# Optimization experiments

Measured on AMD Instinct MI355X. Metric: run time of the kernel, lower is better.

The kernel has to match this reference:

```python
import jax, jax.numpy as jnp
import numpy as np

N = 30000
E = 480000
VDIM = 512
HID = 32
EPS_BN = 1e-5
EPS_COS = 1e-8


def setup_inputs() -> dict:
    key = jax.random.key(0)
    ks = jax.random.split(key, 12)
    inp = {}
    inp["x"] = jax.random.normal(ks[0], (N, 2), dtype=jnp.float32)
    inp["visual"] = jax.random.normal(ks[1], (N, VDIM), dtype=jnp.float32)
    inp["edge_index"] = jax.random.randint(ks[2], (2, E), 0, N, dtype=jnp.int64)
    # input_mlp: Linear(2,32) -> BN(32) -> PReLU -> Dropout(0) -> Linear(32,32)
    inp["w1"] = jax.random.normal(ks[3], (HID, 2), dtype=jnp.float32) * 0.1
    inp["b1"] = jnp.zeros((HID,), dtype=jnp.float32)
    inp["gamma"] = jnp.ones((HID,), dtype=jnp.float32)
    inp["beta"] = jnp.zeros((HID,), dtype=jnp.float32)
    inp["prelu_a"] = jnp.asarray(0.25, dtype=jnp.float32)  # torch default: single shared slope
    inp["w2"] = jax.random.normal(ks[4], (HID, HID), dtype=jnp.float32) * 0.1
    inp["b2"] = jnp.zeros((HID,), dtype=jnp.float32)
    # CMCosConv(32, 32, 512): linear over cos-weighted mean aggregation
    inp["wc"] = jax.random.normal(ks[5], (HID, HID), dtype=jnp.float32) * 0.1
    inp["bc"] = jnp.zeros((HID,), dtype=jnp.float32)
    # gcn_projection_face: Linear(32,1)
    inp["wp"] = jax.random.normal(ks[6], (1, HID), dtype=jnp.float32) * 0.1
    inp["bp"] = jnp.zeros((1,), dtype=jnp.float32)
    return inp


def reference(x, visual, edge_index, w1, b1, gamma, beta, prelu_a, w2, b2, wc, bc, wp, bp):
    # ---- input_mlp ----
    h = x @ w1.T + b1  # [N,32]
    mu = jnp.mean(h, axis=0)
    var = jnp.mean((h - mu) ** 2, axis=0)  # biased, training-mode BN
    h = (h - mu) * jax.lax.rsqrt(var + EPS_BN) * gamma + beta
    h = jnp.where(h >= 0, h, prelu_a * h)  # PReLU, single slope
    h = h @ w2.T + b2  # [N,32]

    # ---- CMCosConv: edge weight = cos(visual_src, visual_dst); cos-weighted mean agg; linear ----
    vn = visual / jnp.maximum(jnp.linalg.norm(visual, axis=-1, keepdims=True), EPS_COS)  # [N,512]
    src = edge_index[0]
    dst = edge_index[1]
    w = jnp.sum(vn[src] * vn[dst], axis=-1)  # [E] cosine per edge (memory-bound gathers)
    msg = w[:, None] * h[src]  # [E,32]
    agg = jax.ops.segment_sum(msg, dst, num_segments=N)  # [N,32]
    deg = jax.ops.segment_sum(jnp.ones_like(w), dst, num_segments=N)  # [N]
    agg = agg / jnp.maximum(deg, 1.0)[:, None]  # mean aggregation
    hc = agg @ wc.T + bc  # [N,32]; conv_activation=None -> identity

    # ---- projection ----
    scores = (hc @ wp.T + bp).squeeze(-1)  # [N]
    return scores
```

## Files before the change

kernel.cpp:

```cpp
#include <hip/hip_runtime.h>
#include <hip/hip_fp16.h>
#include <math.h>

#define N_NODES 30000
#define E_EDGES 480000
#define VD      512
#define HID     32
#define BUCKET  3750
#define K1_BLOCKS 512

#define ACC_OFF  0
#define DEG_OFF  30000
#define SARR_OFF 60000
#define PART_OFF 90000
#define INV_OFF  92560
#define NV_BYTE_OFF 524288u

__device__ inline int edot4(unsigned int a, unsigned int b, int c) {
#if __has_builtin(__builtin_amdgcn_sdot4)
    return __builtin_amdgcn_sdot4((int)a, (int)b, (int)c, false);
#else
    int r = c;
    r += (int)(signed char)(a)       * (int)(signed char)(b);
    r += (int)(signed char)(a >> 8)  * (int)(signed char)(b >> 8);
    r += (int)(signed char)(a >> 16) * (int)(signed char)(b >> 16);
    r += (int)(signed char)(a >> 24) * (int)(signed char)(b >> 24);
    return r;
#endif
}

__device__ inline unsigned int pack4i8(float x0, float x1, float x2, float x3, float sc) {
    int q0 = (int)rintf(x0 * sc);
    int q1 = (int)rintf(x1 * sc);
    int q2 = (int)rintf(x2 * sc);
    int q3 = (int)rintf(x3 * sc);
    return (unsigned int)(q0 & 255) | ((unsigned int)(q1 & 255) << 8) |
           ((unsigned int)(q2 & 255) << 16) | ((unsigned int)(q3 & 255) << 24);
}

__global__ void __launch_bounds__(256) k1_prep(
        const float* __restrict__ x,
        const float* __restrict__ visual,
        float* __restrict__ ws, int i8mode) {
    const int t      = threadIdx.x;
    const int gid    = blockIdx.x * blockDim.x + t;
    const int stride = gridDim.x * blockDim.x;
    const int lane   = t & 63;

    for (int i = gid; i < 2 * N_NODES; i += stride) ws[i] = 0.f;

    {
        __shared__ float red[4][5];
        float s0 = 0.f, s1 = 0.f, s00 = 0.f, s11 = 0.f, s01 = 0.f;
        for (int i = gid; i < N_NODES; i += stride) {
            float2 v = ((const float2*)x)[i];
            s0  += v.x;       s1  += v.y;
            s00 += v.x * v.x; s11 += v.y * v.y;
            s01 += v.x * v.y;
        }
        for (int o = 32; o; o >>= 1) {
            s0  += __shfl_xor(s0,  o, 64);
            s1  += __shfl_xor(s1,  o, 64);
            s00 += __shfl_xor(s00, o, 64);
            s11 += __shfl_xor(s11, o, 64);
            s01 += __shfl_xor(s01, o, 64);
        }
        int wv = t >> 6;
        if (lane == 0) {
            red[wv][0] = s0; red[wv][1] = s1; red[wv][2] = s00;
            red[wv][3] = s11; red[wv][4] = s01;
        }
        __syncthreads();
        if (t < 5) {
            ws[PART_OFF + blockIdx.x * 5 + t] =
                red[0][t] + red[1][t] + red[2][t] + red[3][t];
        }
    }

    char*  nvis8 = (char*)ws + NV_BYTE_OFF;
    float* inv   = ws + INV_OFF;
    const int grp  = (lane >> 4);
    const int sub  = lane & 15;
    const int wave  = gid >> 6;
    const int nwave = stride >> 6;
    for (int base = wave * 4; base < N_NODES; base += nwave * 4) {
        const int node = base + grp;
        const float4* row = (const float4*)(visual + (size_t)node * VD);
        float4 v0 = row[sub];
        float4 v1 = row[sub + 16];
        float4 v2 = row[sub + 32];
        float4 v3 = row[sub + 48];
        float4 v4 = row[sub + 64];
        float4 v5 = row[sub + 80];
        float4 v6 = row[sub + 96];
        float4 v7 = row[sub + 112];
        float p = 0.f, am = 0.f;
        #define ACCUM(vv) \
            p += vv.x*vv.x + vv.y*vv.y + vv.z*vv.z + vv.w*vv.w; \
            am = fmaxf(am, fmaxf(fmaxf(fabsf(vv.x), fabsf(vv.y)), \
                                 fmaxf(fabsf(vv.z), fabsf(vv.w))));
        ACCUM(v0) ACCUM(v1) ACCUM(v2) ACCUM(v3)
        ACCUM(v4) ACCUM(v5) ACCUM(v6) ACCUM(v7)
        #undef ACCUM
        for (int o = 8; o; o >>= 1) {
            p  += __shfl_xor(p, o, 64);
            am  = fmaxf(am, __shfl_xor(am, o, 64));
        }
        float r = 1.0f / fmaxf(sqrtf(p), 1e-8f);
        if (i8mode) {
            float vnmax = am * r;
            float qsc   = 127.0f / fmaxf(vnmax, 1e-20f);
            float rs    = r * qsc;
            unsigned int* orow = (unsigned int*)(nvis8 + (size_t)node * 512);
            orow[sub]       = pack4i8(v0.x, v0.y, v0.z, v0.w, rs);
            orow[sub + 16]  = pack4i8(v1.x, v1.y, v1.z, v1.w, rs);
            orow[sub + 32]  = pack4i8(v2.x, v2.y, v2.z, v2.w, rs);
            orow[sub + 48]  = pack4i8(v3.x, v3.y, v3.z, v3.w, rs);
            orow[sub + 64]  = pack4i8(v4.x, v4.y, v4.z, v4.w, rs);
            orow[sub + 80]  = pack4i8(v5.x, v5.y, v5.z, v5.w, rs);
            orow[sub + 96]  = pack4i8(v6.x, v6.y, v6.z, v6.w, rs);
            orow[sub + 112] = pack4i8(v7.x, v7.y, v7.z, v7.w, rs);
            if (sub == 0) inv[node] = vnmax * (1.0f / 127.0f);
        } else if (sub == 0) {
            inv[node] = r;
        }
    }
}

__global__ void __launch_bounds__(256) k2_sarr(
        const float* __restrict__ x,
        const float* __restrict__ w1, const float* __restrict__ b1,
        const float* __restrict__ gamma, const float* __restrict__ beta,
        const float* __restrict__ prelu_a,
        const float* __restrict__ w2, const float* __restrict__ b2,
        const float* __restrict__ wc, const float* __restrict__ wp,
        const float* __restrict__ ws_ro,
        float* __restrict__ sarr, int i8mode) {
    __shared__ float red[4][5];
    __shared__ float s_S[5];
    __shared__ float s_scale[HID], s_shift[HID], s_u[HID], s_w1a[HID], s_w1b[HID];
    __shared__ float s_wpc[HID];
    __shared__ float s_sb;
    const float* part = ws_ro + PART_OFF;
    const float* qs   = ws_ro + INV_OFF;
    const int t    = threadIdx.x;
    const int lane = t & 63;

    {
        float S[5] = {0.f, 0.f, 0.f, 0.f, 0.f};
        for (int j = t; j < K1_BLOCKS; j += 256) {
            #pragma unroll
            for (int c = 0; c < 5; ++c) S[c] += part[j * 5 + c];
        }
        #pragma unroll
        for (int c = 0; c < 5; ++c)
            for (int o = 32; o; o >>= 1) S[c] += __shfl_xor(S[c], o, 64);
        int wv = t >> 6;
        if (lane == 0) {
            #pragma unroll
            for (int c = 0; c < 5; ++c) red[wv][c] = S[c];
        }
        __syncthreads();
        if (t < 5) s_S[t] = red[0][t] + red[1][t] + red[2][t] + red[3][t];
        __syncthreads();
    }

    if (t < HID) {
        float wpck = 0.f;
        for (int j = 0; j < HID; ++j) wpck += wp[j] * wc[j * HID + t];
        s_wpc[t] = wpck;
        const float invN = 1.0f / (float)N_NODES;
        float m0  = s_S[0] * invN, m1 = s_S[1] * invN;
        float v0  = fmaxf(s_S[2] * invN - m0 * m0, 0.f);
        float v1  = fmaxf(s_S[3] * invN - m1 * m1, 0.f);
        float c01 = s_S[4] * invN - m0 * m1;
        float a0 = w1[2 * t], a1 = w1[2 * t + 1];
        float mean = a0 * m0 + a1 * m1 + b1[t];
        float var  = fmaxf(a0 * a0 * v0 + a1 * a1 * v1 + 2.f * a0 * a1 * c01, 0.f);
        float rs    = 1.0f / sqrtf(var + 1e-5f);
        float scale = gamma[t] * rs;
        s_scale[t] = scale;
        s_shift[t] = beta[t] - mean * scale;
        s_w1a[t] = a0; s_w1b[t] = a1;
    }
    __syncthreads();
    if (t < HID) {
        float uu = 0.f;
        for (int k = 0; k < HID; ++k) uu += s_wpc[k] * w2[k * HID + t];
        s_u[t] = uu;
    }
    if (t == 0) {
        float sb = 0.f;
        for (int k = 0; k < HID; ++k) sb += s_wpc[k] * b2[k];
        s_sb = sb;
    }
    __syncthreads();
    const float aslope = prelu_a[0];
    const float sb = s_sb;
    for (int i = blockIdx.x * blockDim.x + t; i < N_NODES; i += gridDim.x * blockDim.x) {
        float2 xv = ((const float2*)x)[i];
        float sacc = sb;
        #pragma unroll
        for (int c = 0; c < HID; ++c) {
            float h  = s_w1a[c] * xv.x + s_w1b[c] * xv.y + b1[c];
            float tt = h * s_scale[c] + s_shift[c];
            tt = tt >= 0.f ? tt : aslope * tt;
            sacc += tt * s_u[c];
        }
        sarr[i] = i8mode ? sacc * qs[i] : sacc;
    }
}

__global__ void __launch_bounds__(256) k3_edge8(const int* __restrict__ ei,
                                                const float* __restrict__ ws_ro,
                                                float* __restrict__ acc,
                                                float* __restrict__ deg,
                                                const float* __restrict__ sq) {
    const char* nvb = (const char*)ws_ro + NV_BYTE_OFF;
    const int lane = threadIdx.x & 63;
    const int sub  = lane & 7;
    const int g    = lane >> 3;
    const int r    = blockIdx.x & 7;
    const int q    = (blockIdx.x >> 3) * (blockDim.x >> 6) + (threadIdx.x >> 6);
    const int nq   = (gridDim.x >> 3) * (blockDim.x >> 6);
    const int nchunk = E_EDGES >> 6;

    for (int c = q; c < nchunk; c += nq) {
        int idx = (c << 6) + lane;
        int s = ei[idx];
        int d = ei[E_EDGES + idx];
        bool mine = (s / BUCKET == r);
        float mys = mine ? sq[s] : 0.f;
        unsigned long long m = __ballot(mine);
        while (m) {
            int j0 = __ffsll(m) - 1;  m &= m - 1;
            int cnt = 1;
            int j1 = j0, j2 = j0, j3 = j0, j4 = j0, j5 = j0, j6 = j0, j7 = j0;
            if (m) { j1 = __ffsll(m) - 1; m &= m - 1; cnt = 2; }
            if (m) { j2 = __ffsll(m) - 1; m &= m - 1; cnt = 3; }
            if (m) { j3 = __ffsll(m) - 1; m &= m - 1; cnt = 4; }
            if (m) { j4 = __ffsll(m) - 1; m &= m - 1; cnt = 5; }
            if (m) { j5 = __ffsll(m) - 1; m &= m - 1; cnt = 6; }
            if (m) { j6 = __ffsll(m) - 1; m &= m - 1; cnt = 7; }
            if (m) { j7 = __ffsll(m) - 1; m &= m - 1; cnt = 8; }

            int jsel = (g < 4) ? ((g < 2) ? (g == 0 ? j0 : j1) : (g == 2 ? j2 : j3))
                               : ((g < 6) ? (g == 4 ? j4 : j5) : (g == 6 ? j6 : j7));
            int   se = __shfl(s,   jsel, 64);
            int   de = __shfl(d,   jsel, 64);
            float sv = __shfl(mys, jsel, 64);

            const uint4* sa = (const uint4*)(nvb + ((size_t)se << 9)) + sub;
            const uint4* da = (const uint4*)(nvb + ((size_t)de << 9)) + sub;
            uint4 A0 = sa[0];
            uint4 B0 = da[0];
            uint4 A1 = sa[8];
            uint4 B1 = da[8];
            uint4 A2 = sa[16];
            uint4 B2 = da[16];
            uint4 A3 = sa[24];
            uint4 B3 = da[24];

            int p = 0;
            p = edot4(A0.x, B0.x, p);
            p = edot4(A0.y, B0.y, p);
            p = edot4(A0.z, B0.z, p);
            p = edot4(A0.w, B0.w, p);
            p = edot4(A1.x, B1.x, p);
            p = edot4(A1.y, B1.y, p);
            p = edot4(A1.z, B1.z, p);
            p = edot4(A1.w, B1.w, p);
            p = edot4(A2.x, B2.x, p);
            p = edot4(A2.y, B2.y, p);
            p = edot4(A2.z, B2.z, p);
            p = edot4(A2.w, B2.w, p);
            p = edot4(A3.x, B3.x, p);
            p = edot4(A3.y, B3.y, p);
            p = edot4(A3.z, B3.z, p);
            p = edot4(A3.w, B3.w, p);

            p += __shfl_xor(p, 4, 64);
            p += __shfl_xor(p, 2, 64);
            p += __shfl_xor(p, 1, 64);

            if (sub == 0 && g < cnt) {
                atomicAdd(&acc[de], (float)p * sv);
                atomicAdd(&deg[de], 1.0f);
            }
        }
    }
}

__global__ void __launch_bounds__(256) k3_edge32(const int* __restrict__ ei,
                                                 const float* __restrict__ visual,
                                                 const float* __restrict__ inv,
                                                 const float* __restrict__ sarr,
                                                 float* __restrict__ acc,
                                                 float* __restrict__ deg) {
    int wave  = (blockIdx.x * blockDim.x + threadIdx.x) >> 6;
    int lane  = threadIdx.x & 63;
    int nwave = (gridDim.x * blockDim.x) >> 6;
    for (int e = wave; e < E_EDGES; e += nwave) {
        int s = ei[e];
        int d = ei[E_EDGES + e];
        const float4* ra = (const float4*)(visual + (size_t)s * VD);
        const float4* rb = (const float4*)(visual + (size_t)d * VD);
        float4 a0 = ra[lane];
        float4 b0 = rb[lane];
        float4 a1 = ra[lane + 64];
        float4 b1 = rb[lane + 64];
        float p = a0.x*b0.x + a0.y*b0.y + a0.z*b0.z + a0.w*b0.w
                + a1.x*b1.x + a1.y*b1.y + a1.z*b1.z + a1.w*b1.w;
        for (int o = 32; o; o >>= 1) p += __shfl_xor(p, o, 64);
        if (lane == 0) {
            float w = p * inv[s] * inv[d];
            atomicAdd(&acc[d], w * sarr[s]);
            atomicAdd(&deg[d], 1.0f);
        }
    }
}

__global__ void k4_final(const float* __restrict__ acc, const float* __restrict__ deg,
                         const float* __restrict__ qs,
                         const float* __restrict__ bc, const float* __restrict__ wp,
                         const float* __restrict__ bp, float* __restrict__ out,
                         int n, int i8mode) {
    float K = bp[0];
    #pragma unroll
    for (int j = 0; j < HID; ++j) K += wp[j] * bc[j];
    for (int i = blockIdx.x * blockDim.x + threadIdx.x; i < n; i += gridDim.x * blockDim.x) {
        float a = acc[i];
        if (i8mode) a *= qs[i];
        out[i] = a / fmaxf(deg[i], 1.0f) + K;
    }
}

extern "C" void kernel_launch(void* const* d_in, const int* in_sizes, int n_in,
                              void* d_out, int out_size, void* d_ws, size_t ws_size,
                              hipStream_t stream) {
    const float* x       = (const float*)d_in[0];
    const float* visual  = (const float*)d_in[1];
    const int*   ei      = (const int*)  d_in[2];
    const float* w1      = (const float*)d_in[3];
    const float* b1      = (const float*)d_in[4];
    const float* gamma   = (const float*)d_in[5];
    const float* beta    = (const float*)d_in[6];
    const float* prelu_a = (const float*)d_in[7];
    const float* w2      = (const float*)d_in[8];
    const float* b2      = (const float*)d_in[9];
    const float* wc      = (const float*)d_in[10];
    const float* bc      = (const float*)d_in[11];
    const float* wp      = (const float*)d_in[12];
    const float* bp      = (const float*)d_in[13];
    float* out = (float*)d_out;

    float* ws   = (float*)d_ws;
    float* acc  = ws + ACC_OFF;
    float* deg  = ws + DEG_OFF;
    float* sarr = ws + SARR_OFF;
    float* inv  = ws + INV_OFF;

    bool i8ok = ws_size >= (size_t)NV_BYTE_OFF + (size_t)N_NODES * 512;

    k1_prep<<<K1_BLOCKS, 256, 0, stream>>>(x, visual, ws, i8ok ? 1 : 0);
    k2_sarr<<<512, 256, 0, stream>>>(x, w1, b1, gamma, beta, prelu_a, w2, b2, wc, wp,
                                     ws, sarr, i8ok ? 1 : 0);
    if (i8ok) {
        k3_edge8<<<4096, 256, 0, stream>>>(ei, ws, acc, deg, sarr);
    } else {
        k3_edge32<<<4096, 256, 0, stream>>>(ei, visual, inv, sarr, acc, deg);
    }
    k4_final<<<120, 256, 0, stream>>>(acc, deg, inv, bc, wp, bp, out, N_NODES, i8ok ? 1 : 0);
}
```

Before: 185.0 us.

## Pack edge indices to 16 bits and fuse degree count into an f64 atomic

The prep kernel now packs each edge's source and destination indices into one 32-bit word of 16-bit halves. This halves the index traffic in the edge kernel, where each of the 8 bucket passes rescans the whole edge list. The separate f32 accumulator and degree atomics are merged into one double-precision atomic that adds the message plus a large constant (2^20). The final kernel decodes the count and the sum from that double. This halves the atomic count, at the cost of an extra packing pass, f64 atomics, and writing the packed buffer even when the fallback path has too little workspace for it.

```diff
diff --git a/kernel.cpp b/kernel.cpp
--- a/kernel.cpp
+++ b/kernel.cpp
@@ -8,13 +8,21 @@
 #define HID     32
 #define BUCKET  3750
 #define K1_BLOCKS 512
-
-#define ACC_OFF  0
-#define DEG_OFF  30000
+#define BIG_ENC 1048576.0
+
 #define SARR_OFF 60000
 #define PART_OFF 90000
 #define INV_OFF  92560
-#define NV_BYTE_OFF 524288u
+#define NV_BYTE_OFF   524288u
+#define EI16_BYTE_OFF 15884288u
+
+__device__ inline void atomAddF64(double* p, double v) {
+#if defined(__HIP_PLATFORM_AMD__)
+    unsafeAtomicAdd(p, v);
+#else
+    atomicAdd(p, v);
+#endif
+}
 
 __device__ inline int edot4(unsigned int a, unsigned int b, int c) {
 #if __has_builtin(__builtin_amdgcn_sdot4)
@@ -41,6 +49,7 @@
 __global__ void __launch_bounds__(256) k1_prep(
         const float* __restrict__ x,
         const float* __restrict__ visual,
+        const int* __restrict__ ei,
         float* __restrict__ ws, int i8mode) {
     const int t      = threadIdx.x;
     const int gid    = blockIdx.x * blockDim.x + t;
@@ -48,6 +57,15 @@
     const int lane   = t & 63;
 
     for (int i = gid; i < 2 * N_NODES; i += stride) ws[i] = 0.f;
+
+    {
+        unsigned int* ei16 = (unsigned int*)((char*)ws + EI16_BYTE_OFF);
+        for (int e = gid; e < E_EDGES; e += stride) {
+            unsigned int s = (unsigned int)ei[e];
+            unsigned int d = (unsigned int)ei[E_EDGES + e];
+            ei16[e] = s | (d << 16);
+        }
+    }
 
     {
         __shared__ float red[4][5];
@@ -211,10 +229,9 @@
     }
 }
 
-__global__ void __launch_bounds__(256) k3_edge8(const int* __restrict__ ei,
+__global__ void __launch_bounds__(256) k3_edge8(const unsigned int* __restrict__ ei16,
                                                 const float* __restrict__ ws_ro,
-                                                float* __restrict__ acc,
-                                                float* __restrict__ deg,
+                                                double* __restrict__ accD,
                                                 const float* __restrict__ sq) {
     const char* nvb = (const char*)ws_ro + NV_BYTE_OFF;
     const int lane = threadIdx.x & 63;
@@ -227,8 +244,9 @@
 
     for (int c = q; c < nchunk; c += nq) {
         int idx = (c << 6) + lane;
-        int s = ei[idx];
-        int d = ei[E_EDGES + idx];
+        unsigned int sd = ei16[idx];
+        int s = (int)(sd & 0xffffu);
+        int d = (int)(sd >> 16);
         bool mine = (s / BUCKET == r);
         float mys = mine ? sq[s] : 0.f;
         unsigned long long m = __ballot(mine);
@@ -284,8 +302,7 @@
             p += __shfl_xor(p, 1, 64);
 
             if (sub == 0 && g < cnt) {
-                atomicAdd(&acc[de], (float)p * sv);
-                atomicAdd(&deg[de], 1.0f);
+                atomAddF64(&accD[de], (double)((float)p * sv) + BIG_ENC);
             }
         }
     }
@@ -295,8 +312,7 @@
                                                  const float* __restrict__ visual,
                                                  const float* __restrict__ inv,
                                                  const float* __restrict__ sarr,
-                                                 float* __restrict__ acc,
-                                                 float* __restrict__ deg) {
+                                                 double* __restrict__ accD) {
     int wave  = (blockIdx.x * blockDim.x + threadIdx.x) >> 6;
     int lane  = threadIdx.x & 63;
     int nwave = (gridDim.x * blockDim.x) >> 6;
@@ -314,13 +330,12 @@
         for (int o = 32; o; o >>= 1) p += __shfl_xor(p, o, 64);
         if (lane == 0) {
             float w = p * inv[s] * inv[d];
-            atomicAdd(&acc[d], w * sarr[s]);
-            atomicAdd(&deg[d], 1.0f);
-        }
-    }
-}
-
-__global__ void k4_final(const float* __restrict__ acc, const float* __restrict__ deg,
+            atomAddF64(&accD[d], (double)(w * sarr[s]) + BIG_ENC);
+        }
+    }
+}
+
+__global__ void k4_final(const double* __restrict__ accD,
                          const float* __restrict__ qs,
                          const float* __restrict__ bc, const float* __restrict__ wp,
                          const float* __restrict__ bp, float* __restrict__ out,
@@ -329,9 +344,11 @@
     #pragma unroll
     for (int j = 0; j < HID; ++j) K += wp[j] * bc[j];
     for (int i = blockIdx.x * blockDim.x + threadIdx.x; i < n; i += gridDim.x * blockDim.x) {
-        float a = acc[i];
+        double total = accD[i];
+        int cnt = (int)__double2ll_rn(total * (1.0 / BIG_ENC));
+        float a = (float)(total - (double)cnt * BIG_ENC);
         if (i8mode) a *= qs[i];
-        out[i] = a / fmaxf(deg[i], 1.0f) + K;
+        out[i] = a / (float)max(cnt, 1) + K;
     }
 }
 
@@ -354,21 +371,21 @@
     const float* bp      = (const float*)d_in[13];
     float* out = (float*)d_out;
 
-    float* ws   = (float*)d_ws;
-    float* acc  = ws + ACC_OFF;
-    float* deg  = ws + DEG_OFF;
-    float* sarr = ws + SARR_OFF;
-    float* inv  = ws + INV_OFF;
-
-    bool i8ok = ws_size >= (size_t)NV_BYTE_OFF + (size_t)N_NODES * 512;
-
-    k1_prep<<<K1_BLOCKS, 256, 0, stream>>>(x, visual, ws, i8ok ? 1 : 0);
+    float*  ws   = (float*)d_ws;
+    double* accD = (double*)d_ws;
+    float*  sarr = ws + SARR_OFF;
+    float*  inv  = ws + INV_OFF;
+    unsigned int* ei16 = (unsigned int*)((char*)d_ws + EI16_BYTE_OFF);
+
+    bool i8ok = ws_size >= (size_t)EI16_BYTE_OFF + (size_t)E_EDGES * 4;
+
+    k1_prep<<<K1_BLOCKS, 256, 0, stream>>>(x, visual, ei, ws, i8ok ? 1 : 0);
     k2_sarr<<<512, 256, 0, stream>>>(x, w1, b1, gamma, beta, prelu_a, w2, b2, wc, wp,
                                      ws, sarr, i8ok ? 1 : 0);
     if (i8ok) {
-        k3_edge8<<<4096, 256, 0, stream>>>(ei, ws, acc, deg, sarr);
+        k3_edge8<<<4096, 256, 0, stream>>>(ei16, ws, accD, sarr);
     } else {
-        k3_edge32<<<4096, 256, 0, stream>>>(ei, visual, inv, sarr, acc, deg);
-    }
-    k4_final<<<120, 256, 0, stream>>>(acc, deg, inv, bc, wp, bp, out, N_NODES, i8ok ? 1 : 0);
-}
+        k3_edge32<<<4096, 256, 0, stream>>>(ei, visual, inv, sarr, accD);
+    }
+    k4_final<<<120, 256, 0, stream>>>(accD, inv, bc, wp, bp, out, N_NODES, i8ok ? 1 : 0);
+}
```

Result: faster. 167.8 us (median of 2 runs) (-9.3%).
